# Performance work log

Measured on AMD Instinct MI355X. Metric: run time of the kernel, lower is better.

The kernel has to match this reference:

```python
import jax, jax.numpy as jnp
import numpy as np

VOXEL_SIZE = np.array([0.1, 0.1, 0.2], np.float32)
PC_RANGE = np.array([-51.2, -51.2, -5.0, 51.2, 51.2, 3.0], np.float32)
MAX_POINTS = 32
MAX_VOXELS = 60000  # training cap (max_voxels[0])
GRID = np.round((PC_RANGE[3:] - PC_RANGE[:3]) / VOXEL_SIZE).astype(np.int64)  # [1024,1024,40]
N_POINTS = 1_200_000


def setup_inputs() -> dict:
    key = jax.random.key(0)
    k1, k2 = jax.random.split(key)
    lo = jnp.asarray(PC_RANGE[:3] - 2.0)   # slight margin -> some out-of-range points get dropped
    hi = jnp.asarray(PC_RANGE[3:] + 2.0)
    xyz = jax.random.uniform(k1, (N_POINTS, 3), minval=lo, maxval=hi)
    feat = jax.random.uniform(k2, (N_POINTS, 1))  # reflectivity
    return {"points": jnp.concatenate([xyz, feat], axis=1)}


def reference(points):
    # Hard voxelization (deterministic): first-occurrence voxel ordering,
    # first max_points points kept per voxel, capped at max_voxels.
    # Outputs padded to static MAX_VOXELS; voxel_num gives the valid count.
    N, ndim = points.shape
    gx, gy, gz = int(GRID[0]), int(GRID[1]), int(GRID[2])
    sentinel = gx * gy * gz  # flat id for out-of-range points (sorts last)

    vs = jnp.asarray(VOXEL_SIZE)
    rmin = jnp.asarray(PC_RANGE[:3])
    c = jnp.floor((points[:, :3] - rmin) / vs).astype(jnp.int32)  # [N,3] (x,y,z)
    valid = jnp.all((c >= 0) & (c < jnp.asarray(GRID, jnp.int32)), axis=1)
    flat = jnp.where(valid, (c[:, 0] * gy + c[:, 1]) * gz + c[:, 2], sentinel)

    # stable sort -> within a voxel, points keep original order
    order = jnp.argsort(flat, stable=True)
    sflat = flat[order]
    svalid = valid[order]

    new_seg = jnp.concatenate([jnp.array([True]), sflat[1:] != sflat[:-1]])
    seg_id = jnp.cumsum(new_seg) - 1                      # segment index per sorted point
    pos = jnp.arange(N)
    seg_start = jax.lax.cummax(jnp.where(new_seg, pos, 0), axis=0)
    rank = pos - seg_start                                # slot of point within its voxel

    seg_rep = jax.ops.segment_min(order, seg_id, num_segments=N)          # first-occurrence point idx
    seg_count = jax.ops.segment_sum(svalid.astype(jnp.int32), seg_id, num_segments=N)
    seg_exists = seg_count > 0                            # real (in-range) voxel segments

    # order voxels by first occurrence (matches deterministic CUDA kernel)
    rep_key = jnp.where(seg_exists, seg_rep, N)
    vox_order = jnp.argsort(rep_key, stable=True)
    vid = jnp.zeros(N, jnp.int32).at[vox_order].set(jnp.arange(N, dtype=jnp.int32))

    # scatter points into [MAX_VOXELS, MAX_POINTS, ndim]
    pv = vid[seg_id]
    keep = svalid & (pv < MAX_VOXELS) & (rank < MAX_POINTS)
    pv_s = jnp.where(keep, pv, MAX_VOXELS)  # OOB -> dropped
    voxels = jnp.zeros((MAX_VOXELS, MAX_POINTS, ndim), points.dtype)
    voxels = voxels.at[pv_s, jnp.minimum(rank, MAX_POINTS - 1)].set(points[order], mode='drop')

    # per-voxel outputs
    seg_vid = jnp.where(seg_exists, vid, MAX_VOXELS)
    npv = jnp.zeros(MAX_VOXELS, jnp.int32).at[seg_vid].set(
        jnp.minimum(seg_count, MAX_POINTS), mode='drop')
    seg_flat = jax.ops.segment_min(sflat, seg_id, num_segments=N)
    zc = seg_flat % gz
    yc = (seg_flat // gz) % gy
    xc = seg_flat // (gy * gz)
    coors = jnp.zeros((MAX_VOXELS, 3), jnp.int32).at[seg_vid].set(
        jnp.stack([zc, yc, xc], axis=1).astype(jnp.int32), mode='drop')  # (z, y, x) like mmcv

    voxel_num = jnp.minimum(jnp.sum(seg_exists.astype(jnp.int32)), MAX_VOXELS)
    return voxels, coors, npv, voxel_num
```

## Files before the change

kernel.cpp:

```cpp
#include <hip/hip_runtime.h>
#include <stdint.h>


#define GX 1024
#define GY 1024
#define GZ 40
#define MAXV 60000
#define MAXP 32
#define HBITS 21
#define HSIZE (1u << HBITS)
#define HMASK (HSIZE - 1u)
#define CANDBIT (1 << 30)
#define FLATMASK (CANDBIT - 1)
#define TB 256
#define EMPTY64 0xFFFFFFFFFFFFFFFFull

#define OFF_COORS ((size_t)MAXV * MAXP * 4)
#define OFF_NPV   (OFF_COORS + (size_t)MAXV * 3)
#define OFF_VNUM  (OFF_NPV + (size_t)MAXV)

typedef unsigned long long u64;

__device__ __forceinline__ unsigned hashf(int flat) {
    return ((unsigned)flat * 2654435761u) >> (32 - HBITS);
}

__global__ void k_init(u64* __restrict__ h64, unsigned char* __restrict__ contested,
                       int* __restrict__ dupcnt, int* __restrict__ repidx,
                       int n, float* __restrict__ oF) {
    int i = blockIdx.x * blockDim.x + threadIdx.x;
    int stride = gridDim.x * blockDim.x;
    for (int j = i; j < (int)HSIZE; j += stride) h64[j] = EMPTY64;
    int nw = (n + 3) / 4;
    unsigned* c4 = (unsigned*)contested;
    for (int j = i; j < nw; j += stride) c4[j] = 0;
    for (int j = i; j < MAXV; j += stride) { dupcnt[j] = 0; repidx[j] = -1; }
    for (int j = i; j < MAXV * 3; j += stride) oF[OFF_COORS + j] = 0.f;
}

__device__ __forceinline__ int voxel_flat(float4 pt) {
    float fx = floorf((pt.x + 51.2f) / 0.1f);
    float fy = floorf((pt.y + 51.2f) / 0.1f);
    float fz = floorf((pt.z + 5.0f) / 0.2f);
    int cx = (int)fx, cy = (int)fy, cz = (int)fz;
    bool valid = (fx >= 0.f) & (cx < GX) & (fy >= 0.f) & (cy < GY) & (fz >= 0.f) & (cz < GZ);
    return valid ? (cx * GY + cy) * GZ + cz : -1;
}

__global__ __launch_bounds__(TB) void k_build(const float4* __restrict__ pts, int n,
                                              u64* __restrict__ h64,
                                              int* __restrict__ pflat,
                                              unsigned char* __restrict__ contested) {
    int p = blockIdx.x * blockDim.x + threadIdx.x;
    if (p >= n) return;
    float4 pt = pts[p];
    int flat = voxel_flat(pt);
    if (flat < 0) { pflat[p] = -1; return; }
    u64 want = ((u64)(unsigned)flat << 32) | (unsigned)p;
    unsigned slot = hashf(flat);
    int cand = 0;
    for (int probe = 0; probe < 4096; probe++) {
        u64 cur = atomicCAS(&h64[slot], EMPTY64, want);
        if (cur == EMPTY64) { cand = 1; break; }
        if ((unsigned)(cur >> 32) == (unsigned)flat) {
            if ((unsigned)cur > (unsigned)p) {
                u64 old = atomicMin(&h64[slot], want);
                unsigned oldrep = (unsigned)old;
                if (oldrep > (unsigned)p) {
                    contested[oldrep] = 1;
                    cand = 1;
                }
            }
            break;
        }
        slot = (slot + 1u) & HMASK;
    }
    pflat[p] = flat | (cand ? CANDBIT : 0);
}

__global__ __launch_bounds__(TB) void k_flags(const int* __restrict__ pflat,
                                              const unsigned char* __restrict__ contested,
                                              int n, u64* __restrict__ flagbits,
                                              int* __restrict__ partials) {
    __shared__ int ws[4];
    int b = blockIdx.x, t = threadIdx.x;
    int i = b * TB + t;
    int pred = 0;
    if (i < n) {
        int pf = pflat[i];
        pred = (pf >= 0) && (pf & CANDBIT) && !contested[i];
    }
    u64 m = __ballot(pred);
    int w = t >> 6, lane = t & 63;
    if (lane == 0) { flagbits[b * 4 + w] = m; ws[w] = __popcll(m); }
    __syncthreads();
    if (t == 0) partials[b] = ws[0] + ws[1] + ws[2] + ws[3];
}

__global__ __launch_bounds__(1024) void k_scan(int* __restrict__ partials, int npart,
                                               float* __restrict__ oF) {
    __shared__ int sh[1024];
    int t = threadIdx.x;
    int v[5];
    int s = 0;
    #pragma unroll
    for (int k = 0; k < 5; k++) {
        int idx = t * 5 + k;
        v[k] = (idx < npart) ? partials[idx] : 0;
        s += v[k];
    }
    sh[t] = s;
    __syncthreads();
    for (int off = 1; off < 1024; off <<= 1) {
        int add = (t >= off) ? sh[t - off] : 0;
        __syncthreads();
        sh[t] += add;
        __syncthreads();
    }
    int run = sh[t] - s;
    #pragma unroll
    for (int k = 0; k < 5; k++) {
        int idx = t * 5 + k;
        if (idx < npart) partials[idx] = run;
        run += v[k];
    }
    if (t == 1023) {
        int total = sh[1023];
        if (total > MAXV) total = MAXV;
        oF[OFF_VNUM] = (float)total;
    }
}

__global__ __launch_bounds__(TB) void k_finish(const u64* __restrict__ flagbits,
                                               const int* __restrict__ partials,
                                               const int* __restrict__ pflat,
                                               const u64* __restrict__ h64,
                                               int* __restrict__ repidx,
                                               int* __restrict__ dupcnt,
                                               int* __restrict__ list, int n,
                                               float* __restrict__ oF) {
    int b = blockIdx.x, t = threadIdx.x;
    int i = b * TB + t;
    if (i >= n) return;
    int lane = t & 63, w = t >> 6;
    u64 w0 = flagbits[b * 4 + 0];
    u64 w1 = flagbits[b * 4 + 1];
    u64 w2 = flagbits[b * 4 + 2];
    u64 w3 = flagbits[b * 4 + 3];
    u64 myw = (w == 0) ? w0 : (w == 1) ? w1 : (w == 2) ? w2 : w3;
    int bit = (int)((myw >> lane) & 1);
    int pf = pflat[i];
    if (bit) {
        int wbase = (w > 0 ? __popcll(w0) : 0) + (w > 1 ? __popcll(w1) : 0)
                  + (w > 2 ? __popcll(w2) : 0);
        int vid = partials[b] + wbase + (int)__popcll(myw & ((1ull << lane) - 1ull));
        if (vid < MAXV) {
            int flat = pf & FLATMASK;
            int zc = flat % GZ;
            int t2 = flat / GZ;
            int yc = t2 % GY;
            int xc = t2 / GY;
            size_t cOff = OFF_COORS + (size_t)vid * 3;
            oF[cOff + 0] = (float)zc;
            oF[cOff + 1] = (float)yc;
            oF[cOff + 2] = (float)xc;
            repidx[vid] = i;
        }
    } else if (pf >= 0) {
        int flat = pf & FLATMASK;
        unsigned slot = hashf(flat);
        unsigned rep = 0xFFFFFFFFu;
        for (int probe = 0; probe < 4096; probe++) {
            u64 cur = h64[slot];
            if ((unsigned)(cur >> 32) == (unsigned)flat) { rep = (unsigned)cur; break; }
            if (cur == EMPTY64) break;
            slot = (slot + 1u) & HMASK;
        }
        if (rep != 0xFFFFFFFFu) {
            int br = (int)(rep >> 8);
            int lb = (int)(rep & 255u);
            int dvid = partials[br];
            int wb = br * 4, nw = lb >> 6;
            for (int q = 0; q < nw; q++) dvid += (int)__popcll(flagbits[wb + q]);
            int tail = lb & 63;
            if (tail) dvid += (int)__popcll(flagbits[wb + nw] & ((1ull << tail) - 1ull));
            if (dvid < MAXV) {
                int pos = atomicAdd(&dupcnt[dvid], 1);
                if (pos < MAXP - 1) list[dvid * (MAXP - 1) + pos] = i;
            }
        }
    }
}

__global__ __launch_bounds__(TB) void k_emit(const float4* __restrict__ pts,
                                             const int* __restrict__ repidx,
                                             const int* __restrict__ dupcnt,
                                             const int* __restrict__ list,
                                             float4* __restrict__ outVox,
                                             float* __restrict__ oF) {
    int gid = blockIdx.x * TB + threadIdx.x;
    int vid = gid >> 5;
    if (vid >= MAXV) return;
    int r = gid & 31;
    int ri = repidx[vid];
    int dc = dupcnt[vid];
    int d = dc < (MAXP - 1) ? dc : (MAXP - 1);
    int m = (ri >= 0) ? (1 + d) : 0;
    if (r == 0) oF[OFF_NPV + vid] = (float)m;
    float4 row = make_float4(0.f, 0.f, 0.f, 0.f);
    if (r == 0 && m > 0) {
        row = pts[ri];
    } else if (r < m) {
        const int* lst = &list[vid * (MAXP - 1)];
        int target = r - 1, pick = -1;
        for (int a = 0; a < d; a++) {
            int e = lst[a];
            int rk = 0;
            for (int bq = 0; bq < d; bq++) rk += (lst[bq] < e);
            if (rk == target) pick = e;
        }
        row = pts[pick];
    }
    outVox[(size_t)vid * MAXP + r] = row;
}

extern "C" void kernel_launch(void* const* d_in, const int* in_sizes, int n_in,
                              void* d_out, int out_size, void* d_ws, size_t ws_size,
                              hipStream_t stream) {
    int n = in_sizes[0] / 4;
    const float4* pts = (const float4*)d_in[0];

    int tb = TB;
    int nbp = (n + tb - 1) / tb;
    int nwords = nbp * 4;

    char* base = (char*)d_ws;
    size_t o = 0;
    int* partials = (int*)(base + o);  o += ((size_t)nbp * 4 + 255) & ~(size_t)255;
    int* dupcnt   = (int*)(base + o);  o += (size_t)MAXV * 4;
    int* repidx   = (int*)(base + o);  o += (size_t)MAXV * 4;
    o = (o + 255) & ~(size_t)255;
    u64* flagbits = (u64*)(base + o);  o += (size_t)nwords * 8;
    o = (o + 255) & ~(size_t)255;
    unsigned char* contested = (unsigned char*)(base + o);  o += ((size_t)n + 255) & ~(size_t)255;
    u64* h64      = (u64*)(base + o);  o += (size_t)HSIZE * 8;
    int* pflat    = (int*)(base + o);  o += (size_t)n * 4;
    int* list     = (int*)(base + o);  o += (size_t)MAXV * (MAXP - 1) * 4;

    float* oF = (float*)d_out;

    k_init<<<2048, tb, 0, stream>>>(h64, contested, dupcnt, repidx, n, oF);
    k_build<<<nbp, tb, 0, stream>>>(pts, n, h64, pflat, contested);
    k_flags<<<nbp, tb, 0, stream>>>(pflat, contested, n, flagbits, partials);
    k_scan<<<1, 1024, 0, stream>>>(partials, nbp, oF);
    k_finish<<<nbp, tb, 0, stream>>>(flagbits, partials, pflat, h64, repidx, dupcnt, list, n, oF);
    k_emit<<<(MAXV * MAXP + tb - 1) / tb, tb, 0, stream>>>(pts, repidx, dupcnt, list,
                                                           (float4*)d_out, oF);
}
```

Baseline: 138.8 us.

## Split hash build into early counted pass and read-only late pass

Hash insertion is split into two kernels. The first inserts the first KEARLY points and atomically counts newly created voxels. If that count already reaches MAXV, no voxel first seen later can make the output, so the second kernel only does read-only probes to tag late points in existing voxels and drops the rest. Otherwise it falls back to normal insertion. This removes most atomic CAS traffic and hash-table growth for the bulk of points, at the cost of an extra launch and a global counter read.

```diff
diff --git a/kernel.cpp b/kernel.cpp
--- a/kernel.cpp
+++ b/kernel.cpp
@@ -13,6 +13,7 @@
 #define CANDBIT (1 << 30)
 #define FLATMASK (CANDBIT - 1)
 #define TB 256
+#define KEARLY 131072
 #define EMPTY64 0xFFFFFFFFFFFFFFFFull
 
 #define OFF_COORS ((size_t)MAXV * MAXP * 4)
@@ -27,9 +28,10 @@
 
 __global__ void k_init(u64* __restrict__ h64, unsigned char* __restrict__ contested,
                        int* __restrict__ dupcnt, int* __restrict__ repidx,
-                       int n, float* __restrict__ oF) {
+                       int n, float* __restrict__ oF, int* __restrict__ nvox) {
     int i = blockIdx.x * blockDim.x + threadIdx.x;
     int stride = gridDim.x * blockDim.x;
+    if (i == 0) *nvox = 0;
     for (int j = i; j < (int)HSIZE; j += stride) h64[j] = EMPTY64;
     int nw = (n + 3) / 4;
     unsigned* c4 = (unsigned*)contested;
@@ -47,21 +49,15 @@
     return valid ? (cx * GY + cy) * GZ + cz : -1;
 }
 
-__global__ __launch_bounds__(TB) void k_build(const float4* __restrict__ pts, int n,
-                                              u64* __restrict__ h64,
-                                              int* __restrict__ pflat,
-                                              unsigned char* __restrict__ contested) {
-    int p = blockIdx.x * blockDim.x + threadIdx.x;
-    if (p >= n) return;
-    float4 pt = pts[p];
-    int flat = voxel_flat(pt);
-    if (flat < 0) { pflat[p] = -1; return; }
+__device__ __forceinline__ int build_insert(int p, int flat, u64* __restrict__ h64,
+                                            unsigned char* __restrict__ contested,
+                                            int* __restrict__ nvox, int count_wins) {
     u64 want = ((u64)(unsigned)flat << 32) | (unsigned)p;
     unsigned slot = hashf(flat);
-    int cand = 0;
+    int cand = 0, won = 0;
     for (int probe = 0; probe < 4096; probe++) {
         u64 cur = atomicCAS(&h64[slot], EMPTY64, want);
-        if (cur == EMPTY64) { cand = 1; break; }
+        if (cur == EMPTY64) { cand = 1; won = 1; break; }
         if ((unsigned)(cur >> 32) == (unsigned)flat) {
             if ((unsigned)cur > (unsigned)p) {
                 u64 old = atomicMin(&h64[slot], want);
@@ -75,7 +71,46 @@
         }
         slot = (slot + 1u) & HMASK;
     }
-    pflat[p] = flat | (cand ? CANDBIT : 0);
+    if (count_wins && won) atomicAdd(nvox, 1);
+    return flat | (cand ? CANDBIT : 0);
+}
+
+__global__ __launch_bounds__(TB) void k_build_early(const float4* __restrict__ pts, int nE,
+                                                    u64* __restrict__ h64,
+                                                    int* __restrict__ pflat,
+                                                    unsigned char* __restrict__ contested,
+                                                    int* __restrict__ nvox) {
+    int p = blockIdx.x * blockDim.x + threadIdx.x;
+    if (p >= nE) return;
+    float4 pt = pts[p];
+    int flat = voxel_flat(pt);
+    if (flat < 0) { pflat[p] = -1; return; }
+    pflat[p] = build_insert(p, flat, h64, contested, nvox, 1);
+}
+
+__global__ __launch_bounds__(TB) void k_build_late(const float4* __restrict__ pts, int n,
+                                                   u64* __restrict__ h64,
+                                                   int* __restrict__ pflat,
+                                                   unsigned char* __restrict__ contested,
+                                                   int* __restrict__ nvox) {
+    int p = KEARLY + blockIdx.x * blockDim.x + threadIdx.x;
+    if (p >= n) return;
+    float4 pt = pts[p];
+    int flat = voxel_flat(pt);
+    if (flat < 0) { pflat[p] = -1; return; }
+    if (*nvox >= MAXV) {
+        unsigned slot = hashf(flat);
+        int out = -1;
+        for (int probe = 0; probe < 4096; probe++) {
+            u64 cur = h64[slot];
+            if (cur == EMPTY64) break;
+            if ((unsigned)(cur >> 32) == (unsigned)flat) { out = flat; break; }
+            slot = (slot + 1u) & HMASK;
+        }
+        pflat[p] = out;
+        return;
+    }
+    pflat[p] = build_insert(p, flat, h64, contested, nvox, 0);
 }
 
 __global__ __launch_bounds__(TB) void k_flags(const int* __restrict__ pflat,
@@ -246,11 +281,20 @@
     u64* h64      = (u64*)(base + o);  o += (size_t)HSIZE * 8;
     int* pflat    = (int*)(base + o);  o += (size_t)n * 4;
     int* list     = (int*)(base + o);  o += (size_t)MAXV * (MAXP - 1) * 4;
+    o = (o + 255) & ~(size_t)255;
+    int* nvox     = (int*)(base + o);  o += 256;
 
     float* oF = (float*)d_out;
 
-    k_init<<<2048, tb, 0, stream>>>(h64, contested, dupcnt, repidx, n, oF);
-    k_build<<<nbp, tb, 0, stream>>>(pts, n, h64, pflat, contested);
+    int nE = n < KEARLY ? n : KEARLY;
+    int nbE = (nE + tb - 1) / tb;
+    int nL = n - nE;
+
+    k_init<<<2048, tb, 0, stream>>>(h64, contested, dupcnt, repidx, n, oF, nvox);
+    k_build_early<<<nbE, tb, 0, stream>>>(pts, nE, h64, pflat, contested, nvox);
+    if (nL > 0)
+        k_build_late<<<(nL + tb - 1) / tb, tb, 0, stream>>>(pts, n, h64, pflat,
+                                                            contested, nvox);
     k_flags<<<nbp, tb, 0, stream>>>(pflat, contested, n, flagbits, partials);
     k_scan<<<1, 1024, 0, stream>>>(partials, nbp, oF);
     k_finish<<<nbp, tb, 0, stream>>>(flagbits, partials, pflat, h64, repidx, dupcnt, list, n, oF);
```

Result: faster. 135.1 us (median of 2 runs) (-2.6%).
